# Optimization experiments

Measured on AMD Instinct MI355X. Metric: run time of the kernel, lower is better.

Reference implementation:

```python
import jax, jax.numpy as jnp
import numpy as np

HOP = 256
B, F, NB = 16, 4096, 65

def setup_inputs() -> dict:
    key = jax.random.key(0)
    k1, k2 = jax.random.split(key)
    filter_bank = jax.random.normal(k1, (B, F, NB), dtype=jnp.float32)
    noise_u = jax.random.uniform(k2, (B, F, HOP), dtype=jnp.float32)
    return {"filter_bank": filter_bank, "noise_u": noise_u}

def amp_to_impulse_response(amp, target_size):
    # treat real amp as complex spectrum with zero imag, go to time domain
    amp_c = jax.lax.complex(amp, jnp.zeros_like(amp))
    ir = jnp.fft.irfft(amp_c, axis=-1)            # [B, F, 2*(NB-1)]
    filter_size = ir.shape[-1]
    ir = jnp.roll(ir, filter_size // 2, axis=-1)
    n = jnp.arange(filter_size, dtype=ir.dtype)
    win = 0.5 * (1.0 - jnp.cos(2.0 * jnp.pi * n / filter_size))  # periodic hann (torch default)
    ir = ir * win
    ir = jnp.pad(ir, ((0, 0), (0, 0), (0, target_size - filter_size)))
    ir = jnp.roll(ir, -(filter_size // 2), axis=-1)
    return ir

def fft_convolve(signal, kernel):
    n = signal.shape[-1]
    sig = jnp.pad(signal, ((0, 0), (0, 0), (0, n)))
    ker = jnp.pad(kernel, ((0, 0), (0, 0), (kernel.shape[-1], 0)))
    out = jnp.fft.irfft(jnp.fft.rfft(sig) * jnp.fft.rfft(ker))
    return out[..., out.shape[-1] // 2:]

def reference(filter_bank, noise_u):
    impulse = amp_to_impulse_response(filter_bank, HOP)   # [B, F, HOP]
    noise = noise_u * 2.0 - 1.0                           # [B, F, HOP]
    out = fft_convolve(noise, impulse)                    # [B, F, HOP]
    return out.reshape(out.shape[0], -1, 1)               # [B, F*HOP, 1]
```

## Files before the change

### kernel.cpp

```cpp
#include <hip/hip_runtime.h>
#include <math.h>

#define NB 65
#define HOPS 256
#define RPB 16
#define THREADS 256
#define TAPS_OFF 576
#define RSTRIDE 708

#define PHYS(i) ((i) + (((i) >> 5) << 2))

__global__ __launch_bounds__(THREADS) void noisefilter_kernel(
    const float* __restrict__ fb,
    const float* __restrict__ nz,
    float* __restrict__ out)
{
    __shared__ float lds[RPB * RSTRIDE];
    const int tid = threadIdx.x;
    const int r   = tid >> 4;
    const int l16 = tid & 15;
    const int t0  = l16 << 4;
    const size_t row0 = (size_t)blockIdx.x * RPB;
    float* rowbuf = &lds[r * RSTRIDE];

    const float* fbb = fb + row0 * NB;
    for (int i = tid; i < RPB * NB; i += THREADS) {
        int rr = i / NB;
        int k  = i - rr * NB;
        lds[rr * RSTRIDE + TAPS_OFF + k] = fbb[i];
    }
    __syncthreads();

    float cj[5], s1[5], s2[5];
#pragma unroll
    for (int j = 0; j < 5; ++j) {
        cj[j] = __cosf((float)(l16 + 16 * j) * 0.0490873852123405f );
        s1[j] = 0.0f; s2[j] = 0.0f;
    }
    const float* amp = rowbuf + TAPS_OFF;
    {
        float a = amp[64];
#pragma unroll
        for (int j = 0; j < 5; ++j) {
            float t = a - s2[j];
            float sn = fmaf(cj[j] + cj[j], s1[j], t);
            s2[j] = s1[j]; s1[j] = sn;
        }
    }
#pragma unroll
    for (int kb = 48; kb >= 0; kb -= 16) {
        float ab[16];
#pragma unroll
        for (int x = 0; x < 4; ++x) {
            float4 v = *(const float4*)(amp + kb + 4 * x);
            ab[4*x] = v.x; ab[4*x+1] = v.y; ab[4*x+2] = v.z; ab[4*x+3] = v.w;
        }
#pragma unroll
        for (int kk = 15; kk >= 0; --kk) {
            float a  = ab[kk];
            float a2 = (kb + kk == 0) ? a : a + a;
#pragma unroll
            for (int j = 0; j < 5; ++j) {
                float t = a2 - s2[j];
                float sn = fmaf(cj[j] + cj[j], s1[j], t);
                s2[j] = s1[j]; s1[j] = sn;
            }
        }
    }
    __syncthreads();

#pragma unroll
    for (int j = 0; j < 5; ++j) {
        int nj = l16 + 16 * j;
        if (nj <= 64) {
            float G = s1[j] - cj[j] * s2[j];
            float T = G * (1.0f + cj[j]) * (1.0f / 256.0f);
            rowbuf[TAPS_OFF + nj] = T;
            if (nj >= 1 && nj <= 63) rowbuf[TAPS_OFF + 128 - nj] = T;
        }
    }

#pragma unroll
    for (int x = 0; x < 4; ++x)
        *(float4*)(rowbuf + PHYS(t0 + 4 * x)) = make_float4(0.f, 0.f, 0.f, 0.f);

    const float4* nz4 = (const float4*)(nz + row0 * HOPS);
#pragma unroll
    for (int p = 0; p < 4; ++p) {
        int idx = tid + p * THREADS;
        float4 v = nz4[idx];
        int rr = idx >> 6;
        int o  = ((idx & 63) << 2) + 256;
        *(float4*)(&lds[rr * RSTRIDE + PHYS(o)]) =
            make_float4(fmaf(2.f, v.x, -1.f), fmaf(2.f, v.y, -1.f),
                        fmaf(2.f, v.z, -1.f), fmaf(2.f, v.w, -1.f));
    }
    __syncthreads();

    float f[16];
#pragma unroll
    for (int d = 0; d < 16; ++d) f[d] = 0.f;
#pragma unroll
    for (int ch = 0; ch < 8; ++ch) {
        const int off  = (ch < 4) ? 256 : 128;
        const int base = off + t0 - 16 * ch - 16;
        float w[32];
#pragma unroll
        for (int x = 0; x < 8; ++x) {
            int L = base + 4 * x;
            float4 v = *(const float4*)(rowbuf + PHYS(L));
            w[4*x] = v.x; w[4*x+1] = v.y; w[4*x+2] = v.z; w[4*x+3] = v.w;
        }
        float tp[16];
#pragma unroll
        for (int x = 0; x < 4; ++x) {
            float4 v = *(const float4*)(rowbuf + TAPS_OFF + 16 * ch + 4 * x);
            tp[4*x] = v.x; tp[4*x+1] = v.y; tp[4*x+2] = v.z; tp[4*x+3] = v.w;
        }
#pragma unroll
        for (int kk = 0; kk < 16; ++kk) {
#pragma unroll
            for (int d = 0; d < 16; ++d)
                f[d] = fmaf(tp[kk], w[16 + d - kk], f[d]);
        }
    }

    float* op = out + (row0 + r) * HOPS + t0;
#pragma unroll
    for (int x = 0; x < 4; ++x)
        *(float4*)(op + 4 * x) = make_float4(f[4*x], f[4*x+1], f[4*x+2], f[4*x+3]);
}

extern "C" void kernel_launch(void* const* d_in, const int* in_sizes, int n_in,
                              void* d_out, int out_size, void* d_ws, size_t ws_size,
                              hipStream_t stream) {
    const float* fb = (const float*)d_in[0];
    const float* nz = (const float*)d_in[1];
    float* o = (float*)d_out;
    const int rows = 16 * 4096;
    noisefilter_kernel<<<dim3(rows / RPB), dim3(THREADS), 0, stream>>>(fb, nz, o);
}
```

Before: 175.3 us.

## Exploit IR symmetry, split Goertzel even/odd, halve rows per block, prefetch noise

Halves rows per block and threads, and adds a min-blocks launch bound to raise occupancy. The Goertzel recurrence is split into even and odd tap chains across two frequency groups, using the symmetry of the cosine transform to cut recurrence work. The noise load is issued before the first barrier so it overlaps the filter-bank load. The convolution is restructured so taps 0-63 run on full 16-output tiles and taps 64-127 are computed once and shared through LDS to the threads that need them. This is more complex indexing, with a risk of correctness bugs in the symmetry and correction terms.

```diff
diff --git a/kernel.cpp b/kernel.cpp
--- a/kernel.cpp
+++ b/kernel.cpp
@@ -3,14 +3,41 @@
 
 #define NB 65
 #define HOPS 256
-#define RPB 16
-#define THREADS 256
-#define TAPS_OFF 576
-#define RSTRIDE 708
+#define RPB 8
+#define THREADS 128
+#define TAPS_OFF 360
+#define RSTRIDE 492
 
 #define PHYS(i) ((i) + (((i) >> 5) << 2))
 
-__global__ __launch_bounds__(THREADS) void noisefilter_kernel(
+__device__ __forceinline__ void load16(float (&d)[16], const float* p) {
+#pragma unroll
+    for (int x = 0; x < 4; ++x) {
+        float4 v = *(const float4*)(p + 4 * x);
+        d[4*x] = v.x; d[4*x+1] = v.y; d[4*x+2] = v.z; d[4*x+3] = v.w;
+    }
+}
+__device__ __forceinline__ void load16s(float (&d)[16], const float* rowbuf, int L) {
+#pragma unroll
+    for (int x = 0; x < 4; ++x) {
+        float4 v = *(const float4*)(rowbuf + PHYS(L + 4 * x));
+        d[4*x] = v.x; d[4*x+1] = v.y; d[4*x+2] = v.z; d[4*x+3] = v.w;
+    }
+}
+__device__ __forceinline__ void fma16(float (&f)[16], const float (&tp)[16],
+                                      const float (&lo)[16], const float (&hi)[16]) {
+#pragma unroll
+    for (int kk = 0; kk < 16; ++kk) {
+        float t = tp[kk];
+#pragma unroll
+        for (int d = 0; d < 16; ++d) {
+            int j = 16 + d - kk;
+            f[d] = fmaf(t, (j < 16) ? lo[j] : hi[j - 16], f[d]);
+        }
+    }
+}
+
+__global__ __launch_bounds__(THREADS, 4) void noisefilter_kernel(
     const float* __restrict__ fb,
     const float* __restrict__ nz,
     float* __restrict__ out)
@@ -29,68 +56,93 @@
         int k  = i - rr * NB;
         lds[rr * RSTRIDE + TAPS_OFF + k] = fbb[i];
     }
+
+    const float4* nz4 = (const float4*)(nz + row0 * HOPS);
+    float4 nv[4];
+#pragma unroll
+    for (int p = 0; p < 4; ++p) nv[p] = nz4[tid + p * THREADS];
+
     __syncthreads();
 
-    float cj[5], s1[5], s2[5];
-#pragma unroll
-    for (int j = 0; j < 5; ++j) {
-        cj[j] = __cosf((float)(l16 + 16 * j) * 0.0490873852123405f );
-        s1[j] = 0.0f; s2[j] = 0.0f;
-    }
+    const float alphaA = (float)l16 * 0.04908738521234052f;
+    const float alphaB = alphaA + 0.7853981633974483f;
+    const float cA = __cosf(alphaA), cB = __cosf(alphaB);
+    const float c2A = fmaf(2.0f * cA, cA, -1.0f);
+    const float c2B = fmaf(2.0f * cB, cB, -1.0f);
+    const float k2A = c2A + c2A, k2B = c2B + c2B;
+
+    float eA1=0.f,eA2=0.f,oA1=0.f,oA2=0.f;
+    float eB1=0.f,eB2=0.f,oB1=0.f,oB2=0.f;
+    float s32 = 0.f, a0r = 0.f, a64r;
+
     const float* amp = rowbuf + TAPS_OFF;
     {
         float a = amp[64];
-#pragma unroll
-        for (int j = 0; j < 5; ++j) {
-            float t = a - s2[j];
-            float sn = fmaf(cj[j] + cj[j], s1[j], t);
-            s2[j] = s1[j]; s1[j] = sn;
-        }
+        a64r = a;
+        { float t = a - eA2; float s = fmaf(k2A, eA1, t); eA2 = eA1; eA1 = s; }
+        { float t = a - eB2; float s = fmaf(k2B, eB1, t); eB2 = eB1; eB1 = s; }
+        s32 += a;
     }
 #pragma unroll
     for (int kb = 48; kb >= 0; kb -= 16) {
         float ab[16];
-#pragma unroll
-        for (int x = 0; x < 4; ++x) {
-            float4 v = *(const float4*)(amp + kb + 4 * x);
-            ab[4*x] = v.x; ab[4*x+1] = v.y; ab[4*x+2] = v.z; ab[4*x+3] = v.w;
-        }
+        load16(ab, amp + kb);
 #pragma unroll
         for (int kk = 15; kk >= 0; --kk) {
-            float a  = ab[kk];
-            float a2 = (kb + kk == 0) ? a : a + a;
-#pragma unroll
-            for (int j = 0; j < 5; ++j) {
-                float t = a2 - s2[j];
-                float sn = fmaf(cj[j] + cj[j], s1[j], t);
-                s2[j] = s1[j]; s1[j] = sn;
+            float a = ab[kk];
+            if (kk & 1) {
+                { float t = a - oA2; float s = fmaf(k2A, oA1, t); oA2 = oA1; oA1 = s; }
+                { float t = a - oB2; float s = fmaf(k2B, oB1, t); oB2 = oB1; oB1 = s; }
+            } else {
+                { float t = a - eA2; float s = fmaf(k2A, eA1, t); eA2 = eA1; eA1 = s; }
+                { float t = a - eB2; float s = fmaf(k2B, eB1, t); eB2 = eB1; eB1 = s; }
+                if ((kk >> 1) & 1) s32 -= a; else s32 += a;
             }
         }
-    }
-    __syncthreads();
-
-#pragma unroll
-    for (int j = 0; j < 5; ++j) {
-        int nj = l16 + 16 * j;
-        if (nj <= 64) {
-            float G = s1[j] - cj[j] * s2[j];
-            float T = G * (1.0f + cj[j]) * (1.0f / 256.0f);
-            rowbuf[TAPS_OFF + nj] = T;
-            if (nj >= 1 && nj <= 63) rowbuf[TAPS_OFF + 128 - nj] = T;
-        }
-    }
-
-#pragma unroll
-    for (int x = 0; x < 4; ++x)
-        *(float4*)(rowbuf + PHYS(t0 + 4 * x)) = make_float4(0.f, 0.f, 0.f, 0.f);
-
-    const float4* nz4 = (const float4*)(nz + row0 * HOPS);
+        if (kb == 0) a0r = ab[0];
+    }
+
+    const float EA = fmaf(-c2A, eA2, eA1);
+    const float OA = cA * (oA1 - oA2);
+    const float EB = fmaf(-c2B, eB2, eB1);
+    const float OB = cB * (oB1 - oB2);
+    const float pm = (l16 & 1) ? -1.f : 1.f;
+    const float corr = fmaf(pm, a64r, a0r);
+    const float inv = 1.0f / 256.0f;
+    float* tps = rowbuf + TAPS_OFF;
+
+    {
+        float GA  = fmaf(2.f, EA + OA, -corr);
+        float GAm = fmaf(2.f, EA - OA, -corr);
+        float TA  = GA  * (1.0f + cA) * inv;
+        float TAm = GAm * (1.0f - cA) * inv;
+        tps[l16] = TA;
+        tps[64 - l16] = TAm;
+        if (l16 >= 1) { tps[128 - l16] = TA; tps[64 + l16] = TAm; }
+    }
+    {
+        float GB  = fmaf(2.f, EB + OB, -corr);
+        float GBm = fmaf(2.f, EB - OB, -corr);
+        float TB  = GB  * (1.0f + cB) * inv;
+        float TBm = GBm * (1.0f - cB) * inv;
+        tps[16 + l16] = TB;  tps[112 - l16] = TB;
+        tps[48 - l16] = TBm; tps[80 + l16]  = TBm;
+    }
+    {
+        float G32 = fmaf(2.f, s32, -(a0r + a64r));
+        float T32 = G32 * inv;
+        tps[32] = T32;
+        tps[96] = T32;
+    }
+
+    *(float4*)(rowbuf + PHYS(4 * l16)) = make_float4(0.f, 0.f, 0.f, 0.f);
+
 #pragma unroll
     for (int p = 0; p < 4; ++p) {
         int idx = tid + p * THREADS;
-        float4 v = nz4[idx];
+        float4 v = nv[p];
         int rr = idx >> 6;
-        int o  = ((idx & 63) << 2) + 256;
+        int o  = ((idx & 63) << 2) + 64;
         *(float4*)(&lds[rr * RSTRIDE + PHYS(o)]) =
             make_float4(fmaf(2.f, v.x, -1.f), fmaf(2.f, v.y, -1.f),
                         fmaf(2.f, v.z, -1.f), fmaf(2.f, v.w, -1.f));
@@ -100,28 +152,46 @@
     float f[16];
 #pragma unroll
     for (int d = 0; d < 16; ++d) f[d] = 0.f;
-#pragma unroll
-    for (int ch = 0; ch < 8; ++ch) {
-        const int off  = (ch < 4) ? 256 : 128;
-        const int base = off + t0 - 16 * ch - 16;
-        float w[32];
-#pragma unroll
-        for (int x = 0; x < 8; ++x) {
-            int L = base + 4 * x;
-            float4 v = *(const float4*)(rowbuf + PHYS(L));
-            w[4*x] = v.x; w[4*x+1] = v.y; w[4*x+2] = v.z; w[4*x+3] = v.w;
-        }
-        float tp[16];
+    float X[16], Y[16], Z[16], tp[16];
+    {
+        const int b0 = t0 + 48;
+        load16s(X, rowbuf, b0);      load16s(Y, rowbuf, b0 + 16);
+        load16(tp, tps + 0);   fma16(f, tp, X, Y);
+        load16s(Z, rowbuf, b0 - 16);
+        load16(tp, tps + 16);  fma16(f, tp, Z, X);
+        load16s(Y, rowbuf, b0 - 32);
+        load16(tp, tps + 32);  fma16(f, tp, Y, Z);
+        load16s(X, rowbuf, b0 - 48);
+        load16(tp, tps + 48);  fma16(f, tp, X, Y);
+    }
+
+    float g[4] = {0.f, 0.f, 0.f, 0.f};
+#pragma unroll
+    for (int c = 0; c < 4; ++c) {
+        float W[20];
+#pragma unroll
+        for (int x = 0; x < 5; ++x) {
+            float4 v = *(const float4*)(rowbuf + PHYS(48 + 4 * l16 - 16 * c + 4 * x));
+            W[4*x] = v.x; W[4*x+1] = v.y; W[4*x+2] = v.z; W[4*x+3] = v.w;
+        }
+        float tp2[16];
+        load16(tp2, tps + 64 + 16 * c);
+#pragma unroll
+        for (int kk = 0; kk < 16; ++kk) {
+            float t = tp2[kk];
+#pragma unroll
+            for (int d = 0; d < 4; ++d)
+                g[d] = fmaf(t, W[16 + d - kk], g[d]);
+        }
+    }
+    *(float4*)(tps + 64 + 4 * l16) = make_float4(g[0], g[1], g[2], g[3]);
+    if (l16 >= 12) {
+        const float* sc = tps + 64 + ((l16 - 12) << 4);
 #pragma unroll
         for (int x = 0; x < 4; ++x) {
-            float4 v = *(const float4*)(rowbuf + TAPS_OFF + 16 * ch + 4 * x);
-            tp[4*x] = v.x; tp[4*x+1] = v.y; tp[4*x+2] = v.z; tp[4*x+3] = v.w;
-        }
-#pragma unroll
-        for (int kk = 0; kk < 16; ++kk) {
-#pragma unroll
-            for (int d = 0; d < 16; ++d)
-                f[d] = fmaf(tp[kk], w[16 + d - kk], f[d]);
+            float4 v = *(const float4*)(sc + 4 * x);
+            f[4*x]   += v.x; f[4*x+1] += v.y;
+            f[4*x+2] += v.z; f[4*x+3] += v.w;
         }
     }
 
```

Result: faster. 153.3 us (-12.6%).
